# Performance work log

Measured on AMD Instinct MI355X. Metric: run time of the kernel, lower is better.

The kernel has to match this reference:

```python
import jax, jax.numpy as jnp
import numpy as np

N = 100000      # nodes
E = 1250000     # edges
IN = 128        # in_channels
H = 64          # hidden_channels
L = 2           # num_layers (GCNConv count)
EPS = 1e-5      # BatchNorm eps


def setup_inputs() -> dict:
    key = jax.random.key(0)
    ks = jax.random.split(key, 10)
    x = jax.random.normal(ks[0], (N, IN), jnp.float32)
    edge_index = jax.random.randint(ks[1], (2, E), 0, N, dtype=jnp.int32)
    fc_w = jax.random.normal(ks[2], (IN, H), jnp.float32) / np.sqrt(IN)
    fc_b = jax.random.normal(ks[3], (H,), jnp.float32) * 0.01
    conv_w = jax.random.normal(ks[4], (L, H, H), jnp.float32) / np.sqrt(H)
    conv_b = jax.random.normal(ks[5], (L, H), jnp.float32) * 0.01
    bn_gamma = jnp.ones((L + 1, H), jnp.float32)
    bn_beta = jnp.zeros((L + 1, H), jnp.float32)
    bn_mean = jax.random.normal(ks[6], (L + 1, H), jnp.float32) * 0.1
    bn_var = jax.random.uniform(ks[7], (L + 1, H), jnp.float32) + 0.5
    return {"x": x, "edge_index": edge_index, "fc_w": fc_w, "fc_b": fc_b,
            "conv_w": conv_w, "conv_b": conv_b, "bn_gamma": bn_gamma,
            "bn_beta": bn_beta, "bn_mean": bn_mean, "bn_var": bn_var}


def reference(x, edge_index, fc_w, fc_b, conv_w, conv_b, bn_gamma, bn_beta, bn_mean, bn_var):
    n = x.shape[0]
    loops = jnp.arange(n, dtype=edge_index.dtype)
    src = jnp.concatenate([edge_index[0], loops])   # add self-loops (GCNConv default)
    dst = jnp.concatenate([edge_index[1], loops])
    # symmetric normalization: deg computed on destination, norm = d_s^-1/2 * d_d^-1/2
    deg = jax.ops.segment_sum(jnp.ones_like(dst, x.dtype), dst, num_segments=n)
    dis = jax.lax.rsqrt(deg)                        # deg >= 1 thanks to self-loops
    norm = dis[src] * dis[dst]                      # [E+N]

    def bn(h, i):  # eval-mode BatchNorm1d with running stats
        return (h - bn_mean[i]) * (bn_gamma[i] * jax.lax.rsqrt(bn_var[i] + EPS)) + bn_beta[i]

    h = jax.nn.relu(bn(x @ fc_w + fc_b, 0))         # [N, H]; dropout is identity in eval
    last = h
    for i in range(conv_w.shape[0]):
        hw = h @ conv_w[i]                          # GCNConv: transform then aggregate
        agg = jax.ops.segment_sum(hw[src] * norm[:, None], dst, num_segments=n) + conv_b[i]
        h = jax.nn.relu(bn(agg, i + 1)) + last      # residual to post-fc activation
    return h
```

## Files before the change

### kernel.cpp

```cpp
#include <hip/hip_runtime.h>

#define NNODES 100000
#define NEDGES 1250000
#define IN_CH 128
#define HID 64
#define BN_EPS 1e-5f

#define NPAD 100352
#define DRANGE 12500
#define FILL_CHUNK 2048
#define FILL_CHUNKS 611
#define GBLOCKS 6250
#define ELL_C 32
#define OVF_CAP 65536

typedef __attribute__((ext_vector_type(8))) short s16x8;
typedef __attribute__((ext_vector_type(4))) float f32x4;

__device__ __forceinline__ ushort f2bf(float f) {
    union { float f; unsigned int i; } c;
    c.f = f;
    unsigned int lsb = (c.i >> 16) & 1u;
    return (ushort)((c.i + 0x7FFFu + lsb) >> 16);
}
__device__ __forceinline__ float bf2f(ushort u) {
    union { unsigned int i; float f; } c;
    c.i = (unsigned int)u << 16;
    return c.f;
}
__device__ __forceinline__ float asf(unsigned int i) {
    union { unsigned int i; float f; } c;
    c.i = i;
    return c.f;
}

__global__ void csr_zero(int* cnt, int* ovf_n) {
    int i = blockIdx.x * blockDim.x + threadIdx.x;
    if (i < NNODES) cnt[i] = 0;
    if (i == 0) *ovf_n = 0;
}

__global__ void csr_fill(const int* __restrict__ src, const int* __restrict__ dst,
                         int* cnt, int* __restrict__ ell,
                         int* ovf_n, int2* __restrict__ ovf) {
    int p = blockIdx.x & 7;
    int base = (blockIdx.x >> 3) * FILL_CHUNK;
    int lo = p * DRANGE, hi = lo + DRANGE;
#pragma unroll
    for (int k = 0; k < FILL_CHUNK / 256; ++k) {
        int e = base + k * 256 + threadIdx.x;
        if (e < NEDGES) {
            int d = __builtin_nontemporal_load(&dst[e]);
            if (d >= lo && d < hi) {
                int s = __builtin_nontemporal_load(&src[e]);
                int slot = atomicAdd(&cnt[d], 1);
                if (slot < ELL_C) {
                    ell[(d << 5) + slot] = s << 7;
                } else {
                    int oi = atomicAdd(ovf_n, 1);
                    if (oi < OVF_CAP) ovf[oi] = make_int2(d, s << 7);
                }
            }
        }
    }
}

__global__ __launch_bounds__(256) void fc_bn_relu(
        const float* __restrict__ x, const float* __restrict__ w,
        const float* __restrict__ b,
        const float* __restrict__ g, const float* __restrict__ be,
        const float* __restrict__ mu, const float* __restrict__ var,
        const int* __restrict__ cnt, float* __restrict__ dis,
        ushort* __restrict__ h0) {
    const int wave = threadIdx.x >> 6;
    const int lane = threadIdx.x & 63;
    const int m = lane & 15;
    const int q = lane >> 4;
    const int node_base = (blockIdx.x * 4 + wave) * 16;

    if (m == 0) {
#pragma unroll
        for (int r = 0; r < 4; ++r) {
            int node = node_base + q * 4 + r;
            if (node < NNODES) dis[node] = rsqrtf((float)(cnt[node] + 1));
        }
    }

    s16x8 bfrag[4][4];
#pragma unroll
    for (int kc = 0; kc < 4; ++kc)
#pragma unroll
        for (int ct = 0; ct < 4; ++ct)
#pragma unroll
            for (int j = 0; j < 8; ++j)
                bfrag[kc][ct][j] = (short)f2bf(w[(kc * 32 + q * 8 + j) * HID + ct * 16 + m]);

    f32x4 acc[4] = {{0,0,0,0},{0,0,0,0},{0,0,0,0},{0,0,0,0}};

    int row = node_base + m;
    if (row >= NNODES) row = NNODES - 1;
    const float4* xp = (const float4*)(x + (size_t)row * IN_CH + q * 8);

#pragma unroll
    for (int kc = 0; kc < 4; ++kc) {
        float4 a0 = xp[kc * 8 + 0];
        float4 a1 = xp[kc * 8 + 1];
        s16x8 af;
        af[0] = (short)f2bf(a0.x); af[1] = (short)f2bf(a0.y);
        af[2] = (short)f2bf(a0.z); af[3] = (short)f2bf(a0.w);
        af[4] = (short)f2bf(a1.x); af[5] = (short)f2bf(a1.y);
        af[6] = (short)f2bf(a1.z); af[7] = (short)f2bf(a1.w);
#pragma unroll
        for (int ct = 0; ct < 4; ++ct)
            acc[ct] = __builtin_amdgcn_mfma_f32_16x16x32_bf16(af, bfrag[kc][ct], acc[ct], 0, 0, 0);
    }

#pragma unroll
    for (int ct = 0; ct < 4; ++ct) {
        int col = ct * 16 + m;
        float sc = g[col] * rsqrtf(var[col] + BN_EPS);
        float off = (b[col] - mu[col]) * sc + be[col];
#pragma unroll
        for (int r = 0; r < 4; ++r) {
            int node = node_base + q * 4 + r;
            if (node < NNODES)
                h0[(size_t)node * HID + col] =
                    f2bf(fmaxf(acc[ct][r] * sc + off, 0.f));
        }
    }
}

__global__ __launch_bounds__(256) void conv_mm(
        const ushort* __restrict__ h, const float* __restrict__ w,
        const float* __restrict__ dis, ushort* __restrict__ hws) {
    const int wave = threadIdx.x >> 6;
    const int lane = threadIdx.x & 63;
    const int m = lane & 15;
    const int q = lane >> 4;
    const int node_base = (blockIdx.x * 4 + wave) * 16;

    s16x8 bfrag[2][4];
#pragma unroll
    for (int kc = 0; kc < 2; ++kc)
#pragma unroll
        for (int ct = 0; ct < 4; ++ct)
#pragma unroll
            for (int j = 0; j < 8; ++j)
                bfrag[kc][ct][j] = (short)f2bf(w[(kc * 32 + q * 8 + j) * HID + ct * 16 + m]);

    f32x4 acc[4] = {{0,0,0,0},{0,0,0,0},{0,0,0,0},{0,0,0,0}};

    int row = node_base + m;
    if (row >= NNODES) row = NNODES - 1;

#pragma unroll
    for (int kc = 0; kc < 2; ++kc) {
        const s16x8* hp = (const s16x8*)(h + (size_t)row * HID + kc * 32 + q * 8);
        s16x8 af = *hp;
#pragma unroll
        for (int ct = 0; ct < 4; ++ct)
            acc[ct] = __builtin_amdgcn_mfma_f32_16x16x32_bf16(af, bfrag[kc][ct], acc[ct], 0, 0, 0);
    }

    float dv[4];
#pragma unroll
    for (int r = 0; r < 4; ++r) {
        int node = node_base + q * 4 + r;
        dv[r] = (node < NNODES) ? dis[node] : 0.f;
    }
#pragma unroll
    for (int ct = 0; ct < 4; ++ct) {
#pragma unroll
        for (int r = 0; r < 4; ++r) {
            int node = node_base + q * 4 + r;
            if (node < NNODES)
                hws[(size_t)node * HID + ct * 16 + m] = f2bf(acc[ct][r] * dv[r]);
        }
    }
}

__global__ __launch_bounds__(256) void gather_update(
        const ushort* __restrict__ hws,
        const int* __restrict__ cnt, const int* __restrict__ ell,
        const int* __restrict__ ovf_n, const int2* __restrict__ ovf,
        const float* __restrict__ dis,
        const float* __restrict__ bias,
        const float* __restrict__ g, const float* __restrict__ be,
        const float* __restrict__ mu, const float* __restrict__ var,
        const ushort* __restrict__ last,
        ushort* __restrict__ out_bf, float* __restrict__ out_f,
        int write_f32) {
    const int wave = threadIdx.x >> 6;
    const int lane = threadIdx.x & 63;
    const int d = blockIdx.x * 16 + wave * 4 + (lane >> 4);
    const int m = lane & 15;
    const unsigned int moff = (unsigned int)m * 8u;
    const unsigned int doff = ((unsigned int)d << 7) + moff;

    const char* hb = (const char*)hws;

    uint2 sv = *(const uint2*)(hb + doff);
    float a0 = asf(sv.x << 16), a1 = asf(sv.x & 0xffff0000u);
    float a2 = asf(sv.y << 16), a3 = asf(sv.y & 0xffff0000u);

    const int n = cnt[d];
    const int nn = (n < ELL_C) ? n : ELL_C;
    const int* sp = ell + ((size_t)d << 5);

    int k = 0;
    for (; k + 8 <= nn; k += 8) {
        unsigned int o0 = (unsigned int)sp[k + 0] + moff;
        unsigned int o1 = (unsigned int)sp[k + 1] + moff;
        unsigned int o2 = (unsigned int)sp[k + 2] + moff;
        unsigned int o3 = (unsigned int)sp[k + 3] + moff;
        unsigned int o4 = (unsigned int)sp[k + 4] + moff;
        unsigned int o5 = (unsigned int)sp[k + 5] + moff;
        unsigned int o6 = (unsigned int)sp[k + 6] + moff;
        unsigned int o7 = (unsigned int)sp[k + 7] + moff;
        uint2 v0 = *(const uint2*)(hb + o0);
        uint2 v1 = *(const uint2*)(hb + o1);
        uint2 v2 = *(const uint2*)(hb + o2);
        uint2 v3 = *(const uint2*)(hb + o3);
        uint2 v4 = *(const uint2*)(hb + o4);
        uint2 v5 = *(const uint2*)(hb + o5);
        uint2 v6 = *(const uint2*)(hb + o6);
        uint2 v7 = *(const uint2*)(hb + o7);
        a0 += asf(v0.x << 16); a1 += asf(v0.x & 0xffff0000u);
        a2 += asf(v0.y << 16); a3 += asf(v0.y & 0xffff0000u);
        a0 += asf(v1.x << 16); a1 += asf(v1.x & 0xffff0000u);
        a2 += asf(v1.y << 16); a3 += asf(v1.y & 0xffff0000u);
        a0 += asf(v2.x << 16); a1 += asf(v2.x & 0xffff0000u);
        a2 += asf(v2.y << 16); a3 += asf(v2.y & 0xffff0000u);
        a0 += asf(v3.x << 16); a1 += asf(v3.x & 0xffff0000u);
        a2 += asf(v3.y << 16); a3 += asf(v3.y & 0xffff0000u);
        a0 += asf(v4.x << 16); a1 += asf(v4.x & 0xffff0000u);
        a2 += asf(v4.y << 16); a3 += asf(v4.y & 0xffff0000u);
        a0 += asf(v5.x << 16); a1 += asf(v5.x & 0xffff0000u);
        a2 += asf(v5.y << 16); a3 += asf(v5.y & 0xffff0000u);
        a0 += asf(v6.x << 16); a1 += asf(v6.x & 0xffff0000u);
        a2 += asf(v6.y << 16); a3 += asf(v6.y & 0xffff0000u);
        a0 += asf(v7.x << 16); a1 += asf(v7.x & 0xffff0000u);
        a2 += asf(v7.y << 16); a3 += asf(v7.y & 0xffff0000u);
    }
    for (; k + 4 <= nn; k += 4) {
        unsigned int o0 = (unsigned int)sp[k + 0] + moff;
        unsigned int o1 = (unsigned int)sp[k + 1] + moff;
        unsigned int o2 = (unsigned int)sp[k + 2] + moff;
        unsigned int o3 = (unsigned int)sp[k + 3] + moff;
        uint2 v0 = *(const uint2*)(hb + o0);
        uint2 v1 = *(const uint2*)(hb + o1);
        uint2 v2 = *(const uint2*)(hb + o2);
        uint2 v3 = *(const uint2*)(hb + o3);
        a0 += asf(v0.x << 16); a1 += asf(v0.x & 0xffff0000u);
        a2 += asf(v0.y << 16); a3 += asf(v0.y & 0xffff0000u);
        a0 += asf(v1.x << 16); a1 += asf(v1.x & 0xffff0000u);
        a2 += asf(v1.y << 16); a3 += asf(v1.y & 0xffff0000u);
        a0 += asf(v2.x << 16); a1 += asf(v2.x & 0xffff0000u);
        a2 += asf(v2.y << 16); a3 += asf(v2.y & 0xffff0000u);
        a0 += asf(v3.x << 16); a1 += asf(v3.x & 0xffff0000u);
        a2 += asf(v3.y << 16); a3 += asf(v3.y & 0xffff0000u);
    }
    for (; k < nn; ++k) {
        uint2 v = *(const uint2*)(hb + ((unsigned int)sp[k] + moff));
        a0 += asf(v.x << 16); a1 += asf(v.x & 0xffff0000u);
        a2 += asf(v.y << 16); a3 += asf(v.y & 0xffff0000u);
    }
    if (n > ELL_C) {
        int on = *ovf_n;
        if (on > OVF_CAP) on = OVF_CAP;
        for (int j = 0; j < on; ++j) {
            int2 e = ovf[j];
            if (e.x == d) {
                uint2 v = *(const uint2*)(hb + ((unsigned int)e.y + moff));
                a0 += asf(v.x << 16); a1 += asf(v.x & 0xffff0000u);
                a2 += asf(v.y << 16); a3 += asf(v.y & 0xffff0000u);
            }
        }
    }

    float dd = dis[d];
    float4 bi  = ((const float4*)bias)[m];
    float4 gv  = ((const float4*)g)[m];
    float4 bev = ((const float4*)be)[m];
    float4 muv = ((const float4*)mu)[m];
    float4 vav = ((const float4*)var)[m];
    uint2 lv = *(const uint2*)((const char*)last + doff);

    float r0 = fmaxf((a0 * dd + bi.x - muv.x) * (gv.x * rsqrtf(vav.x + BN_EPS)) + bev.x, 0.f)
               + asf(lv.x << 16);
    float r1 = fmaxf((a1 * dd + bi.y - muv.y) * (gv.y * rsqrtf(vav.y + BN_EPS)) + bev.y, 0.f)
               + asf(lv.x & 0xffff0000u);
    float r2 = fmaxf((a2 * dd + bi.z - muv.z) * (gv.z * rsqrtf(vav.z + BN_EPS)) + bev.z, 0.f)
               + asf(lv.y << 16);
    float r3 = fmaxf((a3 * dd + bi.w - muv.w) * (gv.w * rsqrtf(vav.w + BN_EPS)) + bev.w, 0.f)
               + asf(lv.y & 0xffff0000u);

    if (write_f32) {
        ((float4*)out_f)[(size_t)d * 16 + m] = make_float4(r0, r1, r2, r3);
    } else {
        uint2 o;
        o.x = (unsigned int)f2bf(r0) | ((unsigned int)f2bf(r1) << 16);
        o.y = (unsigned int)f2bf(r2) | ((unsigned int)f2bf(r3) << 16);
        *(uint2*)((char*)out_bf + doff) = o;
    }
}

extern "C" void kernel_launch(void* const* d_in, const int* in_sizes, int n_in,
                              void* d_out, int out_size, void* d_ws, size_t ws_size,
                              hipStream_t stream) {
    const float* x      = (const float*)d_in[0];
    const int*   eidx   = (const int*)d_in[1];
    const float* fc_w   = (const float*)d_in[2];
    const float* fc_b   = (const float*)d_in[3];
    const float* conv_w = (const float*)d_in[4];
    const float* conv_b = (const float*)d_in[5];
    const float* bn_g   = (const float*)d_in[6];
    const float* bn_b   = (const float*)d_in[7];
    const float* bn_m   = (const float*)d_in[8];
    const float* bn_v   = (const float*)d_in[9];

    const int* src = eidx;
    const int* dst = eidx + NEDGES;

    float* out = (float*)d_out;

    float*  dis     = (float*)d_ws;
    int*    cnt     = (int*)(dis + NPAD);
    int*    ovf_n   = cnt + NPAD;
    int2*   ovf     = (int2*)(ovf_n + 4);
    int*    ell     = (int*)(ovf + OVF_CAP);
    ushort* h0      = (ushort*)(ell + (size_t)NNODES * ELL_C);
    ushort* h1      = h0 + (size_t)NNODES * HID;
    ushort* hws     = h1 + (size_t)NNODES * HID;

    const int BLK = 256;
    const int gridN   = (NNODES + BLK - 1) / BLK;
    const int gridF   = FILL_CHUNKS * 8;
    const int gridMM  = (NNODES + 63) / 64;

    csr_zero<<<gridN, BLK, 0, stream>>>(cnt, ovf_n);
    csr_fill<<<gridF, BLK, 0, stream>>>(src, dst, cnt, ell, ovf_n, ovf);

    fc_bn_relu<<<gridMM, BLK, 0, stream>>>(x, fc_w, fc_b, bn_g, bn_b, bn_m, bn_v,
                                           cnt, dis, h0);

    conv_mm<<<gridMM, BLK, 0, stream>>>(h0, conv_w, dis, hws);
    gather_update<<<GBLOCKS, BLK, 0, stream>>>(hws, cnt, ell, ovf_n, ovf, dis,
                                               conv_b, bn_g + HID, bn_b + HID,
                                               bn_m + HID, bn_v + HID, h0,
                                               h1, nullptr, 0);

    conv_mm<<<gridMM, BLK, 0, stream>>>(h1, conv_w + HID * HID, dis, hws);
    gather_update<<<GBLOCKS, BLK, 0, stream>>>(hws, cnt, ell, ovf_n, ovf, dis,
                                               conv_b + HID, bn_g + 2 * HID, bn_b + 2 * HID,
                                               bn_m + 2 * HID, bn_v + 2 * HID, h0,
                                               nullptr, out, 1);
}
```

Baseline: 307.5 us.

## Widen gather loads to 16 bytes, vectorize edge reads, replace zero kernel with memset

The gather kernel now assigns 8 lanes per node, each loading 16-byte chunks, instead of 16 lanes loading 8 bytes. This halves the number of memory instructions per neighbor and doubles the nodes handled per block. The CSR fill reads edges as int4 with four edges per thread, and the zeroing kernel is replaced by a hipMemsetAsync over cnt and ovf_n. Wider gathers give fewer lanes per node and so less parallelism per row. The fill loses its nontemporal hints, and the int4 path relies on NEDGES being divisible by 4.

```diff
diff --git a/kernel.cpp b/kernel.cpp
--- a/kernel.cpp
+++ b/kernel.cpp
@@ -8,9 +8,9 @@
 
 #define NPAD 100352
 #define DRANGE 12500
-#define FILL_CHUNK 2048
-#define FILL_CHUNKS 611
-#define GBLOCKS 6250
+#define FILL_CHUNK 4096
+#define FILL_CHUNKS 306
+#define GBLOCKS 3125
 #define ELL_C 32
 #define OVF_CAP 65536
 
@@ -34,33 +34,34 @@
     return c.f;
 }
 
-__global__ void csr_zero(int* cnt, int* ovf_n) {
-    int i = blockIdx.x * blockDim.x + threadIdx.x;
-    if (i < NNODES) cnt[i] = 0;
-    if (i == 0) *ovf_n = 0;
-}
-
 __global__ void csr_fill(const int* __restrict__ src, const int* __restrict__ dst,
                          int* cnt, int* __restrict__ ell,
                          int* ovf_n, int2* __restrict__ ovf) {
     int p = blockIdx.x & 7;
-    int base = (blockIdx.x >> 3) * FILL_CHUNK;
+    int base = (blockIdx.x >> 3) * (FILL_CHUNK / 4);
     int lo = p * DRANGE, hi = lo + DRANGE;
-#pragma unroll
-    for (int k = 0; k < FILL_CHUNK / 256; ++k) {
-        int e = base + k * 256 + threadIdx.x;
-        if (e < NEDGES) {
-            int d = __builtin_nontemporal_load(&dst[e]);
-            if (d >= lo && d < hi) {
-                int s = __builtin_nontemporal_load(&src[e]);
-                int slot = atomicAdd(&cnt[d], 1);
-                if (slot < ELL_C) {
-                    ell[(d << 5) + slot] = s << 7;
-                } else {
-                    int oi = atomicAdd(ovf_n, 1);
-                    if (oi < OVF_CAP) ovf[oi] = make_int2(d, s << 7);
-                }
+    const int4* dst4 = (const int4*)dst;
+    const int4* src4 = (const int4*)src;
+#pragma unroll
+    for (int k = 0; k < FILL_CHUNK / 1024; ++k) {
+        int i = base + k * 256 + threadIdx.x;
+        if (i < NEDGES / 4) {
+            int4 dv = dst4[i];
+            int4 sv = src4[i];
+#define FILL_ONE(D, S)                                                      \
+            if ((D) >= lo && (D) < hi) {                                    \
+                int slot = atomicAdd(&cnt[(D)], 1);                         \
+                if (slot < ELL_C) ell[((D) << 5) + slot] = (S) << 7;        \
+                else {                                                      \
+                    int oi = atomicAdd(ovf_n, 1);                           \
+                    if (oi < OVF_CAP) ovf[oi] = make_int2((D), (S) << 7);   \
+                }                                                           \
             }
+            FILL_ONE(dv.x, sv.x)
+            FILL_ONE(dv.y, sv.y)
+            FILL_ONE(dv.z, sv.z)
+            FILL_ONE(dv.w, sv.w)
+#undef FILL_ONE
         }
     }
 }
@@ -192,16 +193,28 @@
         int write_f32) {
     const int wave = threadIdx.x >> 6;
     const int lane = threadIdx.x & 63;
-    const int d = blockIdx.x * 16 + wave * 4 + (lane >> 4);
-    const int m = lane & 15;
-    const unsigned int moff = (unsigned int)m * 8u;
+    const int grp  = lane >> 3;
+    const int j    = lane & 7;
+    const int d = blockIdx.x * 32 + wave * 8 + grp;
+    const unsigned int moff = (unsigned int)j * 16u;
     const unsigned int doff = ((unsigned int)d << 7) + moff;
 
     const char* hb = (const char*)hws;
 
-    uint2 sv = *(const uint2*)(hb + doff);
-    float a0 = asf(sv.x << 16), a1 = asf(sv.x & 0xffff0000u);
-    float a2 = asf(sv.y << 16), a3 = asf(sv.y & 0xffff0000u);
+    float a[8];
+    {
+        uint4 sv = *(const uint4*)(hb + doff);
+        a[0] = asf(sv.x << 16); a[1] = asf(sv.x & 0xffff0000u);
+        a[2] = asf(sv.y << 16); a[3] = asf(sv.y & 0xffff0000u);
+        a[4] = asf(sv.z << 16); a[5] = asf(sv.z & 0xffff0000u);
+        a[6] = asf(sv.w << 16); a[7] = asf(sv.w & 0xffff0000u);
+    }
+
+#define ACC8(V)                                                         \
+    a[0] += asf((V).x << 16); a[1] += asf((V).x & 0xffff0000u);         \
+    a[2] += asf((V).y << 16); a[3] += asf((V).y & 0xffff0000u);         \
+    a[4] += asf((V).z << 16); a[5] += asf((V).z & 0xffff0000u);         \
+    a[6] += asf((V).w << 16); a[7] += asf((V).w & 0xffff0000u);
 
     const int n = cnt[d];
     const int nn = (n < ELL_C) ? n : ELL_C;
@@ -217,91 +230,80 @@
         unsigned int o5 = (unsigned int)sp[k + 5] + moff;
         unsigned int o6 = (unsigned int)sp[k + 6] + moff;
         unsigned int o7 = (unsigned int)sp[k + 7] + moff;
-        uint2 v0 = *(const uint2*)(hb + o0);
-        uint2 v1 = *(const uint2*)(hb + o1);
-        uint2 v2 = *(const uint2*)(hb + o2);
-        uint2 v3 = *(const uint2*)(hb + o3);
-        uint2 v4 = *(const uint2*)(hb + o4);
-        uint2 v5 = *(const uint2*)(hb + o5);
-        uint2 v6 = *(const uint2*)(hb + o6);
-        uint2 v7 = *(const uint2*)(hb + o7);
-        a0 += asf(v0.x << 16); a1 += asf(v0.x & 0xffff0000u);
-        a2 += asf(v0.y << 16); a3 += asf(v0.y & 0xffff0000u);
-        a0 += asf(v1.x << 16); a1 += asf(v1.x & 0xffff0000u);
-        a2 += asf(v1.y << 16); a3 += asf(v1.y & 0xffff0000u);
-        a0 += asf(v2.x << 16); a1 += asf(v2.x & 0xffff0000u);
-        a2 += asf(v2.y << 16); a3 += asf(v2.y & 0xffff0000u);
-        a0 += asf(v3.x << 16); a1 += asf(v3.x & 0xffff0000u);
-        a2 += asf(v3.y << 16); a3 += asf(v3.y & 0xffff0000u);
-        a0 += asf(v4.x << 16); a1 += asf(v4.x & 0xffff0000u);
-        a2 += asf(v4.y << 16); a3 += asf(v4.y & 0xffff0000u);
-        a0 += asf(v5.x << 16); a1 += asf(v5.x & 0xffff0000u);
-        a2 += asf(v5.y << 16); a3 += asf(v5.y & 0xffff0000u);
-        a0 += asf(v6.x << 16); a1 += asf(v6.x & 0xffff0000u);
-        a2 += asf(v6.y << 16); a3 += asf(v6.y & 0xffff0000u);
-        a0 += asf(v7.x << 16); a1 += asf(v7.x & 0xffff0000u);
-        a2 += asf(v7.y << 16); a3 += asf(v7.y & 0xffff0000u);
+        uint4 v0 = *(const uint4*)(hb + o0);
+        uint4 v1 = *(const uint4*)(hb + o1);
+        uint4 v2 = *(const uint4*)(hb + o2);
+        uint4 v3 = *(const uint4*)(hb + o3);
+        uint4 v4 = *(const uint4*)(hb + o4);
+        uint4 v5 = *(const uint4*)(hb + o5);
+        uint4 v6 = *(const uint4*)(hb + o6);
+        uint4 v7 = *(const uint4*)(hb + o7);
+        ACC8(v0) ACC8(v1) ACC8(v2) ACC8(v3)
+        ACC8(v4) ACC8(v5) ACC8(v6) ACC8(v7)
     }
     for (; k + 4 <= nn; k += 4) {
         unsigned int o0 = (unsigned int)sp[k + 0] + moff;
         unsigned int o1 = (unsigned int)sp[k + 1] + moff;
         unsigned int o2 = (unsigned int)sp[k + 2] + moff;
         unsigned int o3 = (unsigned int)sp[k + 3] + moff;
-        uint2 v0 = *(const uint2*)(hb + o0);
-        uint2 v1 = *(const uint2*)(hb + o1);
-        uint2 v2 = *(const uint2*)(hb + o2);
-        uint2 v3 = *(const uint2*)(hb + o3);
-        a0 += asf(v0.x << 16); a1 += asf(v0.x & 0xffff0000u);
-        a2 += asf(v0.y << 16); a3 += asf(v0.y & 0xffff0000u);
-        a0 += asf(v1.x << 16); a1 += asf(v1.x & 0xffff0000u);
-        a2 += asf(v1.y << 16); a3 += asf(v1.y & 0xffff0000u);
-        a0 += asf(v2.x << 16); a1 += asf(v2.x & 0xffff0000u);
-        a2 += asf(v2.y << 16); a3 += asf(v2.y & 0xffff0000u);
-        a0 += asf(v3.x << 16); a1 += asf(v3.x & 0xffff0000u);
-        a2 += asf(v3.y << 16); a3 += asf(v3.y & 0xffff0000u);
+        uint4 v0 = *(const uint4*)(hb + o0);
+        uint4 v1 = *(const uint4*)(hb + o1);
+        uint4 v2 = *(const uint4*)(hb + o2);
+        uint4 v3 = *(const uint4*)(hb + o3);
+        ACC8(v0) ACC8(v1) ACC8(v2) ACC8(v3)
     }
     for (; k < nn; ++k) {
-        uint2 v = *(const uint2*)(hb + ((unsigned int)sp[k] + moff));
-        a0 += asf(v.x << 16); a1 += asf(v.x & 0xffff0000u);
-        a2 += asf(v.y << 16); a3 += asf(v.y & 0xffff0000u);
+        uint4 v = *(const uint4*)(hb + ((unsigned int)sp[k] + moff));
+        ACC8(v)
     }
     if (n > ELL_C) {
         int on = *ovf_n;
         if (on > OVF_CAP) on = OVF_CAP;
-        for (int j = 0; j < on; ++j) {
-            int2 e = ovf[j];
+        for (int jj = 0; jj < on; ++jj) {
+            int2 e = ovf[jj];
             if (e.x == d) {
-                uint2 v = *(const uint2*)(hb + ((unsigned int)e.y + moff));
-                a0 += asf(v.x << 16); a1 += asf(v.x & 0xffff0000u);
-                a2 += asf(v.y << 16); a3 += asf(v.y & 0xffff0000u);
+                uint4 v = *(const uint4*)(hb + ((unsigned int)e.y + moff));
+                ACC8(v)
             }
         }
     }
+#undef ACC8
 
     float dd = dis[d];
-    float4 bi  = ((const float4*)bias)[m];
-    float4 gv  = ((const float4*)g)[m];
-    float4 bev = ((const float4*)be)[m];
-    float4 muv = ((const float4*)mu)[m];
-    float4 vav = ((const float4*)var)[m];
-    uint2 lv = *(const uint2*)((const char*)last + doff);
-
-    float r0 = fmaxf((a0 * dd + bi.x - muv.x) * (gv.x * rsqrtf(vav.x + BN_EPS)) + bev.x, 0.f)
-               + asf(lv.x << 16);
-    float r1 = fmaxf((a1 * dd + bi.y - muv.y) * (gv.y * rsqrtf(vav.y + BN_EPS)) + bev.y, 0.f)
-               + asf(lv.x & 0xffff0000u);
-    float r2 = fmaxf((a2 * dd + bi.z - muv.z) * (gv.z * rsqrtf(vav.z + BN_EPS)) + bev.z, 0.f)
-               + asf(lv.y << 16);
-    float r3 = fmaxf((a3 * dd + bi.w - muv.w) * (gv.w * rsqrtf(vav.w + BN_EPS)) + bev.w, 0.f)
-               + asf(lv.y & 0xffff0000u);
+    float4 bi0 = ((const float4*)bias)[2 * j], bi1 = ((const float4*)bias)[2 * j + 1];
+    float4 g0  = ((const float4*)g)[2 * j],    g1  = ((const float4*)g)[2 * j + 1];
+    float4 be0 = ((const float4*)be)[2 * j],   be1 = ((const float4*)be)[2 * j + 1];
+    float4 mu0 = ((const float4*)mu)[2 * j],   mu1 = ((const float4*)mu)[2 * j + 1];
+    float4 va0 = ((const float4*)var)[2 * j],  va1 = ((const float4*)var)[2 * j + 1];
+    uint4 lv = *(const uint4*)((const char*)last + doff);
+    float l0 = asf(lv.x << 16), l1 = asf(lv.x & 0xffff0000u);
+    float l2 = asf(lv.y << 16), l3 = asf(lv.y & 0xffff0000u);
+    float l4 = asf(lv.z << 16), l5 = asf(lv.z & 0xffff0000u);
+    float l6 = asf(lv.w << 16), l7 = asf(lv.w & 0xffff0000u);
+
+#define EPI(A, BI, GV, BE, MU, VA, LO) \
+    (fmaxf(((A) * dd + (BI) - (MU)) * ((GV) * rsqrtf((VA) + BN_EPS)) + (BE), 0.f) + (LO))
+    float r0 = EPI(a[0], bi0.x, g0.x, be0.x, mu0.x, va0.x, l0);
+    float r1 = EPI(a[1], bi0.y, g0.y, be0.y, mu0.y, va0.y, l1);
+    float r2 = EPI(a[2], bi0.z, g0.z, be0.z, mu0.z, va0.z, l2);
+    float r3 = EPI(a[3], bi0.w, g0.w, be0.w, mu0.w, va0.w, l3);
+    float r4 = EPI(a[4], bi1.x, g1.x, be1.x, mu1.x, va1.x, l4);
+    float r5 = EPI(a[5], bi1.y, g1.y, be1.y, mu1.y, va1.y, l5);
+    float r6 = EPI(a[6], bi1.z, g1.z, be1.z, mu1.z, va1.z, l6);
+    float r7 = EPI(a[7], bi1.w, g1.w, be1.w, mu1.w, va1.w, l7);
+#undef EPI
 
     if (write_f32) {
-        ((float4*)out_f)[(size_t)d * 16 + m] = make_float4(r0, r1, r2, r3);
+        float4* op = (float4*)(out_f + (size_t)d * HID + j * 8);
+        op[0] = make_float4(r0, r1, r2, r3);
+        op[1] = make_float4(r4, r5, r6, r7);
     } else {
-        uint2 o;
+        uint4 o;
         o.x = (unsigned int)f2bf(r0) | ((unsigned int)f2bf(r1) << 16);
         o.y = (unsigned int)f2bf(r2) | ((unsigned int)f2bf(r3) << 16);
-        *(uint2*)((char*)out_bf + doff) = o;
+        o.z = (unsigned int)f2bf(r4) | ((unsigned int)f2bf(r5) << 16);
+        o.w = (unsigned int)f2bf(r6) | ((unsigned int)f2bf(r7) << 16);
+        *(uint4*)((char*)out_bf + doff) = o;
     }
 }
 
@@ -334,11 +336,11 @@
     ushort* hws     = h1 + (size_t)NNODES * HID;
 
     const int BLK = 256;
-    const int gridN   = (NNODES + BLK - 1) / BLK;
     const int gridF   = FILL_CHUNKS * 8;
     const int gridMM  = (NNODES + 63) / 64;
 
-    csr_zero<<<gridN, BLK, 0, stream>>>(cnt, ovf_n);
+    hipMemsetAsync(cnt, 0, (size_t)NPAD * 4 + 16, stream);
+
     csr_fill<<<gridF, BLK, 0, stream>>>(src, dst, cnt, ell, ovf_n, ovf);
 
     fc_bn_relu<<<gridMM, BLK, 0, stream>>>(x, fc_w, fc_b, bn_g, bn_b, bn_m, bn_v,
```

Measured after the change: 307.6 us. Within noise of the previous version (+0.0%).
